# Kernel optimization log

Measured on AMD Instinct MI355X. Metric: run time of the kernel, lower is better.

Reference implementation:

```python
import jax, jax.numpy as jnp
import numpy as np

DIM = 64
NUM_HEADS = 4
SIGMA_RATIO = 1.0


def setup_inputs() -> dict:
    key = jax.random.key(0)
    ks = jax.random.split(key, 10)
    d = DIM
    s = 0.02
    return {
        "x": jax.random.normal(ks[0], (2, d, 64, 64), dtype=jnp.float32),
        "qkv_w": jax.random.normal(ks[1], (3 * d, d), dtype=jnp.float32) * s,
        "qkv_b": jnp.zeros((3 * d,), dtype=jnp.float32),
        "proj_w": jax.random.normal(ks[2], (d, d), dtype=jnp.float32) * s,
        "proj_b": jnp.zeros((d,), dtype=jnp.float32),
        "g1_w": jax.random.normal(ks[3], (16, 1), dtype=jnp.float32) * 0.5,
        "g1_b": jnp.zeros((16,), dtype=jnp.float32),
        "g2_w": jax.random.normal(ks[4], (NUM_HEADS, 16), dtype=jnp.float32) * 0.5,
        "g2_b": jnp.zeros((NUM_HEADS,), dtype=jnp.float32),
    }


def reference(x, qkv_w, qkv_b, proj_w, proj_b, g1_w, g1_b, g2_w, g2_b):
    B, C, H, W = x.shape
    nh = NUM_HEADS
    hd = C // nh
    N = H * W
    scale = hd ** -0.5

    # edge strength |x[i]-x[i-1]| summed over channels, replicate-padded
    diff_h = jnp.abs(x[:, :, :, 1:] - x[:, :, :, :-1]).sum(axis=1)  # [B,H,W-1]
    diff_v = jnp.abs(x[:, :, 1:, :] - x[:, :, :-1, :]).sum(axis=1)  # [B,H-1,W]
    edge_h = jnp.pad(diff_h, ((0, 0), (0, 0), (0, 1)), mode="edge")
    edge_v = jnp.pad(diff_v, ((0, 0), (0, 1), (0, 0)), mode="edge")
    es = (edge_h + edge_v)[..., None]  # [B,H,W,1]

    # gate MLP: Linear(1,16) -> GELU(exact) -> Linear(16,nh) -> sigmoid
    h1 = jax.nn.gelu(es @ g1_w.T + g1_b, approximate=False)
    gate = jax.nn.sigmoid(h1 @ g2_w.T + g2_b)  # [B,H,W,nh]

    x_seq = x.transpose(0, 2, 3, 1).reshape(B, N, C)
    qkv = (x_seq @ qkv_w.T + qkv_b).reshape(B, N, 3, nh, hd)
    qkv = qkv.transpose(2, 0, 3, 1, 4)  # [3,B,nh,N,hd]
    q, k, v = qkv[0], qkv[1], qkv[2]

    attn = jax.nn.softmax(jnp.einsum("bhnd,bhmd->bhnm", q, k) * scale, axis=-1)

    gate_sender = gate.reshape(B, N, nh).transpose(0, 2, 1)  # [B,nh,N]
    gate_sender = (1.0 - gate_sender * SIGMA_RATIO * 0.1)[..., None]  # [B,nh,N,1]
    attn = attn * gate_sender
    attn = attn / (attn.sum(axis=-1, keepdims=True) + 1e-8)

    out = jnp.einsum("bhnm,bhmd->bnhd", attn, v).reshape(B, N, C)
    out = out @ proj_w.T + proj_b
    return out.reshape(B, H, W, C).transpose(0, 3, 1, 2)
```

## Files before the change

kernel.cpp:

```cpp
#include <hip/hip_runtime.h>
#include <cstdint>


namespace {
constexpr int B  = 2;
constexpr int C  = 64;
constexpr int NH = 4;
constexpr int HD = 16;
constexpr int N  = 4096;
constexpr int MSA = 4;
constexpr int MT  = 256;
constexpr int VROW  = 2 * MT + 16;
constexpr int KSZ   = MT * 32;
constexpr int BUFSZ = KSZ + HD * VROW;

constexpr size_t QKV1     = (size_t)B * NH * N * HD;
constexpr size_t KB_OFF   = QKV1;
constexpr size_t VT_OFF   = 2 * QKV1;
constexpr size_t PO_OFF_U = 3 * QKV1;
constexpr size_t PO_SZ    = (size_t)B * NH * MSA * N * HD;
constexpr size_t PL_OFF_F = (PO_OFF_U + PO_SZ) / 2;
constexpr float QSCALE = 0.36067376022224085f;
}

typedef short bf16x8 __attribute__((ext_vector_type(8)));
typedef float f32x16 __attribute__((ext_vector_type(16)));
typedef int   i32x4  __attribute__((ext_vector_type(4)));

__device__ __forceinline__ unsigned short f2bf(float f) {
  unsigned u = __float_as_uint(f);
  u = (u + 0x7fffu + ((u >> 16) & 1u)) >> 16;
  return (unsigned short)u;
}
__device__ __forceinline__ int cvtpk(float lo, float hi) {
  int r;
  asm("v_cvt_pk_bf16_f32 %0, %1, %2" : "=v"(r) : "v"(lo), "v"(hi));
  return r;
}
__device__ __forceinline__ float fexp2(float x) {
#if __has_builtin(__builtin_amdgcn_exp2f)
  return __builtin_amdgcn_exp2f(x);
#else
  float r;
  asm("v_exp_f32 %0, %1" : "=v"(r) : "v"(x));
  return r;
#endif
}
__device__ __forceinline__ float frcp(float x) {
#if __has_builtin(__builtin_amdgcn_rcpf)
  return __builtin_amdgcn_rcpf(x);
#else
  float r;
  asm("v_rcp_f32 %0, %1" : "=v"(r) : "v"(x));
  return r;
#endif
}
__device__ __forceinline__ void plswap(int a, int b, int h, int& x, int& y) {
#if __has_builtin(__builtin_amdgcn_permlane32_swap)
  (void)h;
  auto r = __builtin_amdgcn_permlane32_swap(a, b, false, false);
  x = r[0]; y = r[1];
#else
  const int ea = __shfl_xor(a, 32), eb = __shfl_xor(b, 32);
  x = h ? eb : a;
  y = h ? b : ea;
#endif
}

__global__ __launch_bounds__(256) void qkv_mfma_kernel(
    const float* __restrict__ x, const float* __restrict__ w,
    const float* __restrict__ bias, unsigned short* __restrict__ qb,
    unsigned short* __restrict__ kb, unsigned short* __restrict__ vtb) {
  __shared__ char wl[64 * 128];
  __shared__ char tl[4 * 2048];
  const int tid = threadIdx.x;
  const int lane = tid & 63, wid = tid >> 6;
  const int l31 = lane & 31, h = lane >> 5;
  const int nw = wid >> 1, jw = wid & 1;
  const int b = blockIdx.y, n0 = blockIdx.x * 64, z = blockIdx.z;

#pragma unroll
  for (int k = 0; k < 8; ++k) {
    const int p = tid + k * 256;
    const int j = p >> 5, c2 = (p & 31) * 2;
    const float2 wv = *(const float2*)(w + ((size_t)z * 64 + j) * 64 + c2);
    *(int*)(wl + j * 128 + ((2 * c2) ^ ((j & 7) << 4))) = cvtpk(wv.x, wv.y);
  }

  const int nA = n0 + nw * 32 + l31;
  bf16x8 af[4];
#pragma unroll
  for (int kk = 0; kk < 4; ++kk) {
    float e[8];
#pragma unroll
    for (int i = 0; i < 8; ++i)
      e[i] = x[((size_t)b * C + kk * 16 + h * 8 + i) * N + nA];
    i32x4 pk = {cvtpk(e[0], e[1]), cvtpk(e[2], e[3]),
                cvtpk(e[4], e[5]), cvtpk(e[6], e[7])};
    af[kk] = __builtin_bit_cast(bf16x8, pk);
  }
  __syncthreads();

  const int j = jw * 32 + l31;
  f32x16 acc = {};
#pragma unroll
  for (int kk = 0; kk < 4; ++kk) {
    bf16x8 bf =
        *(const bf16x8*)(wl + j * 128 + ((kk * 32 + h * 16) ^ ((j & 7) << 4)));
    acc = __builtin_amdgcn_mfma_f32_32x32x16_bf16(af[kk], bf, acc, 0, 0, 0);
  }
  const float bj = bias[z * 64 + j];
  char* myt = tl + wid * 2048;

  if (z < 2) {
    const float sc = (z == 0) ? QSCALE : 1.0f;
#pragma unroll
    for (int r = 0; r < 16; ++r) {
      const int n = (r & 3) + 8 * (r >> 2) + 4 * h;
      *(unsigned short*)(myt + n * 64 + l31 * 2) = f2bf((acc[r] + bj) * sc);
    }
#pragma unroll
    for (int u = 0; u < 2; ++u) {
      const int chunk = lane * 2 + u;
      const int n = chunk >> 2, c = chunk & 3;
      const uint4 vv = *(const uint4*)(myt + n * 64 + c * 16);
      const int jj = jw * 32 + c * 8;
      const int hh = jj >> 4, half = (jj >> 3) & 1;
      const int bh = b * NH + hh;
      if (z == 0) {
        *(uint4*)(qb + ((size_t)bh * N + n0 + nw * 32 + n) * HD + half * 8) = vv;
      } else {
        const size_t ck = (size_t)bh * 8192 +
                          (size_t)((n0 >> 5) + nw) * 64 + half * 32 + n;
        *(uint4*)(kb + ck * 8) = vv;
      }
    }
  } else {
#pragma unroll
    for (int p = 0; p < 8; ++p) {
      const int r = 2 * p;
      const int n = (r & 3) + 8 * (r >> 2) + 4 * h;
      *(int*)(myt + l31 * 64 + n * 2) = cvtpk(acc[r] + bj, acc[r + 1] + bj);
    }
#pragma unroll
    for (int u = 0; u < 2; ++u) {
      const int chunk = lane * 2 + u;
      const int jj = chunk >> 2, c = chunk & 3;
      const uint4 vv = *(const uint4*)(myt + jj * 64 + c * 16);
      const int vj = jw * 32 + jj;
      const int hh = vj >> 4, hd = vj & 15;
      *(uint4*)(vtb + ((size_t)(b * NH + hh) * HD + hd) * N + n0 + nw * 32 +
                c * 8) = vv;
    }
  }
}

__global__ __launch_bounds__(256, 4) void attn_mfma_kernel(
    const unsigned short* __restrict__ qb, const unsigned short* __restrict__ kb,
    const unsigned short* __restrict__ vtb, unsigned short* __restrict__ part_o,
    float* __restrict__ part_l) {
  __shared__ uint4 ldsq[2 * BUFSZ / 16];
  char* ldsb = (char*)ldsq;
  const int tid  = threadIdx.x;
  const int lane = tid & 63;
  const int wid  = tid >> 6;
  const int l31  = lane & 31;
  const int h    = lane >> 5;
  const int bh = blockIdx.z;
  const int ms = blockIdx.y;
  const int q0 = blockIdx.x * 128 + wid * 32;
  const int m0 = ms * (N / MSA);
  constexpr int nt = (N / MSA) / MT;

  bf16x8 qf;
  {
    const uint4 qv =
        *(const uint4*)(qb + (((size_t)bh * N) + q0 + l31) * HD + h * 8);
    qf = __builtin_bit_cast(bf16x8, qv);
  }
  const unsigned short* kgp = kb + ((size_t)bh * 8192 + (m0 >> 5) * 64) * 8;
  const unsigned short* vgp = vtb + (size_t)bh * HD * N + m0;
  const int d0 = tid >> 5, c0 = tid & 31;
  const int d1 = d0 + 8;

  {
    uint4 k0 = *(const uint4*)(kgp + (size_t)tid * 8);
    uint4 k1 = *(const uint4*)(kgp + (size_t)(tid + 256) * 8);
    uint4 v0 = *(const uint4*)(vgp + (size_t)d0 * N + c0 * 8);
    uint4 v1 = *(const uint4*)(vgp + (size_t)d1 * N + c0 * 8);
    *(uint4*)(ldsb + tid * 16) = k0;
    *(uint4*)(ldsb + (tid + 256) * 16) = k1;
    *(uint4*)(ldsb + KSZ + d0 * VROW + c0 * 16) = v0;
    *(uint4*)(ldsb + KSZ + d1 * VROW + c0 * 16) = v1;
  }
  __syncthreads();

  const int onef = (l31 == HD) ? 0x3F803F80 : 0;
  const i32x4 onev = {onef, onef, onef, onef};
  const bf16x8 vcst = __builtin_bit_cast(bf16x8, onev);

  f32x16 acc = {};
  int cur = 0;
  for (int t = 0; t < nt; ++t) {
    uint4 k0{}, k1{}, v0{}, v1{};
    const bool pre = (t + 1 < nt);
    if (pre) {
      const unsigned short* kt = kgp + (size_t)(t + 1) * 512 * 8;
      const unsigned short* vt = vgp + (t + 1) * MT;
      k0 = *(const uint4*)(kt + (size_t)tid * 8);
      k1 = *(const uint4*)(kt + (size_t)(tid + 256) * 8);
      v0 = *(const uint4*)(vt + (size_t)d0 * N + c0 * 8);
      v1 = *(const uint4*)(vt + (size_t)d1 * N + c0 * 8);
    }
    const char* kbase = ldsb + cur * BUFSZ;
    const char* vbase = kbase + KSZ;

    bf16x8 kf = *(const bf16x8*)(kbase + (h * 32 + l31) * 16);
    f32x16 zv = {};
    f32x16 stn = __builtin_amdgcn_mfma_f32_32x32x16_bf16(kf, qf, zv, 0, 0, 0);

#pragma unroll
    for (int cc = 0; cc < MT / 32; ++cc) {
      const f32x16 st = stn;
      if (cc + 1 < MT / 32) {
        bf16x8 kf2 =
            *(const bf16x8*)(kbase + ((cc + 1) * 64 + h * 32 + l31) * 16);
        stn = __builtin_amdgcn_mfma_f32_32x32x16_bf16(kf2, qf, zv, 0, 0, 0);
      }
      bf16x8 vf1, vf2;
      if (l31 < HD) {
        const char* vrow = vbase + l31 * VROW + cc * 64 + h * 16;
        vf1 = *(const bf16x8*)(vrow);
        vf2 = *(const bf16x8*)(vrow + 32);
      } else {
        vf1 = vcst;
        vf2 = vcst;
      }
      int dw[8];
#pragma unroll
      for (int jj = 0; jj < 8; ++jj)
        dw[jj] = cvtpk(fexp2(st[2 * jj]), fexp2(st[2 * jj + 1]));
      int w0, w1, w2, w3, w4, w5, w6, w7;
      plswap(dw[0], dw[2], h, w0, w2);
      plswap(dw[1], dw[3], h, w1, w3);
      plswap(dw[4], dw[6], h, w4, w6);
      plswap(dw[5], dw[7], h, w5, w7);
      const i32x4 a1 = {w0, w1, w2, w3};
      const i32x4 a2 = {w4, w5, w6, w7};
      acc = __builtin_amdgcn_mfma_f32_32x32x16_bf16(
          __builtin_bit_cast(bf16x8, a1), vf1, acc, 0, 0, 0);
      acc = __builtin_amdgcn_mfma_f32_32x32x16_bf16(
          __builtin_bit_cast(bf16x8, a2), vf2, acc, 0, 0, 0);
    }
    if (pre) {
      char* nb = ldsb + (cur ^ 1) * BUFSZ;
      *(uint4*)(nb + tid * 16) = k0;
      *(uint4*)(nb + (tid + 256) * 16) = k1;
      *(uint4*)(nb + KSZ + d0 * VROW + c0 * 16) = v0;
      *(uint4*)(nb + KSZ + d1 * VROW + c0 * 16) = v1;
    }
    __syncthreads();
    cur ^= 1;
  }

  const size_t pbase = ((size_t)bh * MSA + ms) * N + q0;
  if (l31 == HD) {
#pragma unroll
    for (int r = 0; r < 16; ++r)
      part_l[pbase + (r & 3) + 8 * (r >> 2) + 4 * h] = acc[r];
  }
  char* myt = ldsb + wid * 1024;
  if (l31 < HD) {
#pragma unroll
    for (int r = 0; r < 16; ++r) {
      const int q = (r & 3) + 8 * (r >> 2) + 4 * h;
      *(unsigned short*)(myt + q * 32 + l31 * 2) = f2bf(acc[r]);
    }
  }
  __syncthreads();
  const int qr = lane >> 1, half = lane & 1;
  const uint4 vv = *(const uint4*)(myt + qr * 32 + half * 16);
  *(uint4*)(part_o + (pbase + qr) * HD + half * 8) = vv;
}

__global__ __launch_bounds__(128) void proj_mfma_kernel(
    const unsigned short* __restrict__ part_o, const float* __restrict__ part_l,
    const float* __restrict__ pw, const float* __restrict__ pb,
    float* __restrict__ out) {
  __shared__ char al[32 * 128];
  __shared__ char bl[64 * 128];
  __shared__ char tl[2 * 4096];
  __shared__ float linv[128];
  const int tid = threadIdx.x;
  const int lane = tid & 63, wid = tid >> 6;
  const int l31 = lane & 31, h = lane >> 5;
  const int b = blockIdx.y, n0 = blockIdx.x * 32;

  {
    const int hh = tid >> 5, n = tid & 31;
    const size_t base = ((size_t)(b * NH + hh) * MSA) * N + n0 + n;
    float l = 0.f;
#pragma unroll
    for (int ms = 0; ms < MSA; ++ms) l += part_l[base + (size_t)ms * N];
    linv[tid] = frcp(l);
  }
#pragma unroll
  for (int k = 0; k < 16; ++k) {
    const int p = tid + k * 128;
    const int cR = p >> 5, d2 = (p & 31) * 2;
    const float2 wv = *(const float2*)(pw + cR * 64 + d2);
    *(int*)(bl + cR * 128 + ((2 * d2) ^ ((cR & 7) << 4))) = cvtpk(wv.x, wv.y);
  }
  __syncthreads();

#pragma unroll
  for (int u = 0; u < 2; ++u) {
    const int chunk = tid * 2 + u;
    const int hh = chunk >> 6, half = (chunk >> 5) & 1, n = chunk & 31;
    const unsigned short* src =
        part_o + (((size_t)(b * NH + hh) * MSA) * N + n0 + n) * HD + half * 8;
    float s[8] = {0.f, 0.f, 0.f, 0.f, 0.f, 0.f, 0.f, 0.f};
#pragma unroll
    for (int ms = 0; ms < MSA; ++ms) {
      const uint4 v = *(const uint4*)(src + (size_t)ms * N * HD);
      const unsigned uu[4] = {v.x, v.y, v.z, v.w};
#pragma unroll
      for (int q = 0; q < 4; ++q) {
        s[2 * q]     += __uint_as_float(uu[q] << 16);
        s[2 * q + 1] += __uint_as_float(uu[q] & 0xffff0000u);
      }
    }
    const float iv = linv[hh * 32 + n];
    const i32x4 pk = {cvtpk(s[0] * iv, s[1] * iv), cvtpk(s[2] * iv, s[3] * iv),
                      cvtpk(s[4] * iv, s[5] * iv), cvtpk(s[6] * iv, s[7] * iv)};
    const int d = hh * 16 + half * 8;
    *(i32x4*)(al + n * 128 + ((2 * d) ^ ((n & 7) << 4))) = pk;
  }
  __syncthreads();

  bf16x8 af[4];
#pragma unroll
  for (int kk = 0; kk < 4; ++kk)
    af[kk] = *(const bf16x8*)(al + l31 * 128 +
                              ((kk * 32 + h * 16) ^ ((l31 & 7) << 4)));
  const int c = wid * 32 + l31;
  f32x16 acc = {};
#pragma unroll
  for (int kk = 0; kk < 4; ++kk) {
    bf16x8 bf =
        *(const bf16x8*)(bl + c * 128 + ((kk * 32 + h * 16) ^ ((c & 7) << 4)));
    acc = __builtin_amdgcn_mfma_f32_32x32x16_bf16(af[kk], bf, acc, 0, 0, 0);
  }
  const float bc = pb[c];

  char* myt = tl + wid * 4096;
#pragma unroll
  for (int p = 0; p < 8; ++p) {
    const int r = 2 * p;
    const int n = (r & 3) + 8 * (r >> 2) + 4 * h;
    *(float2*)(myt + l31 * 128 + n * 4) =
        make_float2(acc[r] + bc, acc[r + 1] + bc);
  }
  __syncthreads();
#pragma unroll
  for (int u = 0; u < 4; ++u) {
    const int chunk = lane * 4 + u;
    const int cc = chunk >> 3, cq = chunk & 7;
    const float4 vv = *(const float4*)(myt + cc * 128 + cq * 16);
    *(float4*)(out + ((size_t)b * C + wid * 32 + cc) * N + n0 + cq * 4) = vv;
  }
}

extern "C" void kernel_launch(void* const* d_in, const int* in_sizes, int n_in,
                              void* d_out, int out_size, void* d_ws, size_t ws_size,
                              hipStream_t stream) {
  const float* x      = (const float*)d_in[0];
  const float* qkv_w  = (const float*)d_in[1];
  const float* qkv_b  = (const float*)d_in[2];
  const float* proj_w = (const float*)d_in[3];
  const float* proj_b = (const float*)d_in[4];
  unsigned short* qb     = (unsigned short*)d_ws;
  unsigned short* kb     = qb + KB_OFF;
  unsigned short* vtb    = qb + VT_OFF;
  unsigned short* part_o = qb + PO_OFF_U;
  float* part_l = (float*)d_ws + PL_OFF_F;
  float* out = (float*)d_out;

  qkv_mfma_kernel<<<dim3(N / 64, B, 3), 256, 0, stream>>>(
      x, qkv_w, qkv_b, qb, kb, vtb);
  attn_mfma_kernel<<<dim3(N / 128, MSA, B * NH), 256, 0, stream>>>(
      qb, kb, vtb, part_o, part_l);
  proj_mfma_kernel<<<dim3(N / 32, B), 128, 0, stream>>>(
      part_o, part_l, proj_w, proj_b, out);
}
```

Measured before the change: 35.05 us.

## Load K/V fragments directly from global memory instead of LDS double-buffering

The V tensor is written by the QKV kernel in a new fragment-ready tiled layout (per 32-key chunk, per half, per head-dim row), so the attention kernel can load both K and V MFMA operands straight from global/L2 memory. The LDS double-buffered staging, the per-tile barriers and the large shared allocation are removed, which lowers LDS use and could allow higher occupancy. The trade-off is that each wave now issues its own global loads with no sharing across the 4 waves of a block and no explicit prefetch. Latency hiding relies on unrolling and occupancy.

```diff
diff --git a/kernel.cpp b/kernel.cpp
--- a/kernel.cpp
+++ b/kernel.cpp
@@ -9,10 +9,6 @@
 constexpr int HD = 16;
 constexpr int N  = 4096;
 constexpr int MSA = 4;
-constexpr int MT  = 256;
-constexpr int VROW  = 2 * MT + 16;
-constexpr int KSZ   = MT * 32;
-constexpr int BUFSZ = KSZ + HD * VROW;
 
 constexpr size_t QKV1     = (size_t)B * NH * N * HD;
 constexpr size_t KB_OFF   = QKV1;
@@ -111,6 +107,7 @@
   }
   const float bj = bias[z * 64 + j];
   char* myt = tl + wid * 2048;
+  const int mt32 = (n0 >> 5) + nw;
 
   if (z < 2) {
     const float sc = (z == 0) ? QSCALE : 1.0f;
@@ -130,8 +127,7 @@
       if (z == 0) {
         *(uint4*)(qb + ((size_t)bh * N + n0 + nw * 32 + n) * HD + half * 8) = vv;
       } else {
-        const size_t ck = (size_t)bh * 8192 +
-                          (size_t)((n0 >> 5) + nw) * 64 + half * 32 + n;
+        const size_t ck = (size_t)bh * 8192 + (size_t)mt32 * 64 + half * 32 + n;
         *(uint4*)(kb + ck * 8) = vv;
       }
     }
@@ -149,8 +145,9 @@
       const uint4 vv = *(const uint4*)(myt + jj * 64 + c * 16);
       const int vj = jw * 32 + jj;
       const int hh = vj >> 4, hd = vj & 15;
-      *(uint4*)(vtb + ((size_t)(b * NH + hh) * HD + hd) * N + n0 + nw * 32 +
-                c * 8) = vv;
+      const size_t ck =
+          (((size_t)(b * NH + hh) * 128 + mt32) * 4 + c) * 16 + hd;
+      *(uint4*)(vtb + ck * 8) = vv;
     }
   }
 }
@@ -159,8 +156,7 @@
     const unsigned short* __restrict__ qb, const unsigned short* __restrict__ kb,
     const unsigned short* __restrict__ vtb, unsigned short* __restrict__ part_o,
     float* __restrict__ part_l) {
-  __shared__ uint4 ldsq[2 * BUFSZ / 16];
-  char* ldsb = (char*)ldsq;
+  __shared__ char tl[4 * 1024];
   const int tid  = threadIdx.x;
   const int lane = tid & 63;
   const int wid  = tid >> 6;
@@ -170,7 +166,7 @@
   const int ms = blockIdx.y;
   const int q0 = blockIdx.x * 128 + wid * 32;
   const int m0 = ms * (N / MSA);
-  constexpr int nt = (N / MSA) / MT;
+  constexpr int NIT = (N / MSA) / 32;
 
   bf16x8 qf;
   {
@@ -178,89 +174,44 @@
         *(const uint4*)(qb + (((size_t)bh * N) + q0 + l31) * HD + h * 8);
     qf = __builtin_bit_cast(bf16x8, qv);
   }
-  const unsigned short* kgp = kb + ((size_t)bh * 8192 + (m0 >> 5) * 64) * 8;
-  const unsigned short* vgp = vtb + (size_t)bh * HD * N + m0;
-  const int d0 = tid >> 5, c0 = tid & 31;
-  const int d1 = d0 + 8;
-
-  {
-    uint4 k0 = *(const uint4*)(kgp + (size_t)tid * 8);
-    uint4 k1 = *(const uint4*)(kgp + (size_t)(tid + 256) * 8);
-    uint4 v0 = *(const uint4*)(vgp + (size_t)d0 * N + c0 * 8);
-    uint4 v1 = *(const uint4*)(vgp + (size_t)d1 * N + c0 * 8);
-    *(uint4*)(ldsb + tid * 16) = k0;
-    *(uint4*)(ldsb + (tid + 256) * 16) = k1;
-    *(uint4*)(ldsb + KSZ + d0 * VROW + c0 * 16) = v0;
-    *(uint4*)(ldsb + KSZ + d1 * VROW + c0 * 16) = v1;
-  }
-  __syncthreads();
+  const unsigned short* kp =
+      kb + ((size_t)bh * 8192 + (size_t)(m0 >> 5) * 64 + h * 32 + l31) * 8;
+  const unsigned short* vp =
+      vtb + ((((size_t)bh * 128 + (m0 >> 5)) * 4 + h) * 16 + l31) * 8;
 
   const int onef = (l31 == HD) ? 0x3F803F80 : 0;
   const i32x4 onev = {onef, onef, onef, onef};
   const bf16x8 vcst = __builtin_bit_cast(bf16x8, onev);
 
   f32x16 acc = {};
-  int cur = 0;
-  for (int t = 0; t < nt; ++t) {
-    uint4 k0{}, k1{}, v0{}, v1{};
-    const bool pre = (t + 1 < nt);
-    if (pre) {
-      const unsigned short* kt = kgp + (size_t)(t + 1) * 512 * 8;
-      const unsigned short* vt = vgp + (t + 1) * MT;
-      k0 = *(const uint4*)(kt + (size_t)tid * 8);
-      k1 = *(const uint4*)(kt + (size_t)(tid + 256) * 8);
-      v0 = *(const uint4*)(vt + (size_t)d0 * N + c0 * 8);
-      v1 = *(const uint4*)(vt + (size_t)d1 * N + c0 * 8);
-    }
-    const char* kbase = ldsb + cur * BUFSZ;
-    const char* vbase = kbase + KSZ;
-
-    bf16x8 kf = *(const bf16x8*)(kbase + (h * 32 + l31) * 16);
+#pragma unroll 8
+  for (int cc = 0; cc < NIT; ++cc) {
+    bf16x8 kf = *(const bf16x8*)(kp + (size_t)cc * 512);
     f32x16 zv = {};
-    f32x16 stn = __builtin_amdgcn_mfma_f32_32x32x16_bf16(kf, qf, zv, 0, 0, 0);
-
-#pragma unroll
-    for (int cc = 0; cc < MT / 32; ++cc) {
-      const f32x16 st = stn;
-      if (cc + 1 < MT / 32) {
-        bf16x8 kf2 =
-            *(const bf16x8*)(kbase + ((cc + 1) * 64 + h * 32 + l31) * 16);
-        stn = __builtin_amdgcn_mfma_f32_32x32x16_bf16(kf2, qf, zv, 0, 0, 0);
-      }
-      bf16x8 vf1, vf2;
-      if (l31 < HD) {
-        const char* vrow = vbase + l31 * VROW + cc * 64 + h * 16;
-        vf1 = *(const bf16x8*)(vrow);
-        vf2 = *(const bf16x8*)(vrow + 32);
-      } else {
-        vf1 = vcst;
-        vf2 = vcst;
-      }
-      int dw[8];
-#pragma unroll
-      for (int jj = 0; jj < 8; ++jj)
-        dw[jj] = cvtpk(fexp2(st[2 * jj]), fexp2(st[2 * jj + 1]));
-      int w0, w1, w2, w3, w4, w5, w6, w7;
-      plswap(dw[0], dw[2], h, w0, w2);
-      plswap(dw[1], dw[3], h, w1, w3);
-      plswap(dw[4], dw[6], h, w4, w6);
-      plswap(dw[5], dw[7], h, w5, w7);
-      const i32x4 a1 = {w0, w1, w2, w3};
-      const i32x4 a2 = {w4, w5, w6, w7};
-      acc = __builtin_amdgcn_mfma_f32_32x32x16_bf16(
-          __builtin_bit_cast(bf16x8, a1), vf1, acc, 0, 0, 0);
-      acc = __builtin_amdgcn_mfma_f32_32x32x16_bf16(
-          __builtin_bit_cast(bf16x8, a2), vf2, acc, 0, 0, 0);
-    }
-    if (pre) {
-      char* nb = ldsb + (cur ^ 1) * BUFSZ;
-      *(uint4*)(nb + tid * 16) = k0;
-      *(uint4*)(nb + (tid + 256) * 16) = k1;
-      *(uint4*)(nb + KSZ + d0 * VROW + c0 * 16) = v0;
-      *(uint4*)(nb + KSZ + d1 * VROW + c0 * 16) = v1;
-    }
-    __syncthreads();
-    cur ^= 1;
+    f32x16 st = __builtin_amdgcn_mfma_f32_32x32x16_bf16(kf, qf, zv, 0, 0, 0);
+    bf16x8 vf1, vf2;
+    if (l31 < HD) {
+      vf1 = *(const bf16x8*)(vp + (size_t)cc * 512);
+      vf2 = *(const bf16x8*)(vp + (size_t)cc * 512 + 256);
+    } else {
+      vf1 = vcst;
+      vf2 = vcst;
+    }
+    int dw[8];
+#pragma unroll
+    for (int jj = 0; jj < 8; ++jj)
+      dw[jj] = cvtpk(fexp2(st[2 * jj]), fexp2(st[2 * jj + 1]));
+    int w0, w1, w2, w3, w4, w5, w6, w7;
+    plswap(dw[0], dw[2], h, w0, w2);
+    plswap(dw[1], dw[3], h, w1, w3);
+    plswap(dw[4], dw[6], h, w4, w6);
+    plswap(dw[5], dw[7], h, w5, w7);
+    const i32x4 a1 = {w0, w1, w2, w3};
+    const i32x4 a2 = {w4, w5, w6, w7};
+    acc = __builtin_amdgcn_mfma_f32_32x32x16_bf16(
+        __builtin_bit_cast(bf16x8, a1), vf1, acc, 0, 0, 0);
+    acc = __builtin_amdgcn_mfma_f32_32x32x16_bf16(
+        __builtin_bit_cast(bf16x8, a2), vf2, acc, 0, 0, 0);
   }
 
   const size_t pbase = ((size_t)bh * MSA + ms) * N + q0;
@@ -269,7 +220,7 @@
     for (int r = 0; r < 16; ++r)
       part_l[pbase + (r & 3) + 8 * (r >> 2) + 4 * h] = acc[r];
   }
-  char* myt = ldsb + wid * 1024;
+  char* myt = tl + wid * 1024;
   if (l31 < HD) {
 #pragma unroll
     for (int r = 0; r < 16; ++r) {
```

After: 37.40 us. 1.07x slower.
